# Kernel optimization log

Hardware: AMD Instinct MI355X
Metric: run time of the kernel (lower is better)

The kernel has to match this reference:

```python
import jax, jax.numpy as jnp
import numpy as np

jax.config.update("jax_enable_x64", True)  # original casts to double for covpool/SVD

BN_EPS = 1e-5


def setup_inputs() -> dict:
    key = jax.random.key(0)
    k1, k2 = jax.random.split(key)
    x = jax.random.normal(k1, (64, 2048, 14, 14), dtype=jnp.float32)
    conv_w = jax.random.normal(k2, (256, 2048), dtype=jnp.float32) * 0.02  # 1x1 conv kernel
    bn_gamma = jnp.ones((256,), dtype=jnp.float32)
    bn_beta = jnp.zeros((256,), dtype=jnp.float32)
    return {"x": x, "conv_w": conv_w, "bn_gamma": bn_gamma, "bn_beta": bn_beta}


def reference(x, conv_w, bn_gamma, bn_beta):
    # --- dimension reduction block: 1x1 conv (no bias) + BN (train mode) + ReLU ---
    y = jnp.einsum('oc,bchw->bohw', conv_w, x)  # [B,256,14,14]
    mean = y.mean(axis=(0, 2, 3), keepdims=True)
    var = y.var(axis=(0, 2, 3), keepdims=True)
    y = (y - mean) * jax.lax.rsqrt(var + BN_EPS)
    y = y * bn_gamma[None, :, None, None] + bn_beta[None, :, None, None]
    y = jnp.maximum(y, 0.0)

    # --- Covpool: x @ (I/M - 11^T/M^2) @ x^T, in float64 as original ---
    B, d, h, w = y.shape
    M = h * w
    z = y.reshape(B, d, M).astype(jnp.float64)
    zc = z - z.mean(axis=2, keepdims=True)          # centering == multiplying by I_hat
    cov = jnp.einsum('bim,bjm->bij', zc, zc) / M    # [B,d,d], symmetric PSD

    # --- Eigen decomposition (SVD of symmetric PSD == eigh), clamp tiny eigvals ---
    s, V = jnp.linalg.eigh(cov)                     # s: [B,d], V: [B,d,d]
    eps = jnp.finfo(jnp.float64).eps
    s = jnp.maximum(s, eps)

    # --- Power: matrix square root Q = V sqrt(S) V^T ---
    Q = jnp.einsum('bij,bj,bkj->bik', V, jnp.sqrt(s), V)  # [B,d,d]

    # --- upper-triangular (incl. diag) vectorization, row-major like torch triu ---
    iu = jnp.triu_indices(d)
    q_triv = Q[:, iu[0], iu[1]]                     # [B, d*(d+1)/2]
    return q_triv.astype(jnp.float32)
```

## Files before the change

### kernel.cpp

```cpp
#include <hip/hip_runtime.h>
#include <hip/hip_bf16.h>

static constexpr int B   = 64;
static constexpr int CIN = 2048;
static constexpr int O   = 256;
static constexpr int HW  = 196;
static constexpr int D   = 256;
static constexpr int TRI = 32896;
static constexpr int NQ_COUPLED = 5;
static constexpr size_t NELEM = (size_t)B * D * D;
static constexpr size_t YN    = (size_t)B * O * HW;

typedef unsigned short u16;
typedef unsigned short u16x4 __attribute__((ext_vector_type(4)));
typedef unsigned short u16x8 __attribute__((ext_vector_type(8)));
typedef __bf16         bf16x8 __attribute__((ext_vector_type(8)));
typedef float          f32x4 __attribute__((ext_vector_type(4)));

static __device__ __forceinline__ u16 f2bf(float x) {
    unsigned int u = __float_as_uint(x);
    u += 0x7FFFu + ((u >> 16) & 1u);
    return (u16)(u >> 16);
}
static __device__ __forceinline__ float bf2f(u16 h) {
    return __uint_as_float(((unsigned int)h) << 16);
}
static __device__ __forceinline__ f32x4 mm_bf16(u16x8 a, u16x8 b, f32x4 c) {
    return __builtin_amdgcn_mfma_f32_16x16x32_bf16(
        __builtin_bit_cast(bf16x8, a), __builtin_bit_cast(bf16x8, b), c, 0, 0, 0);
}

__global__ __launch_bounds__(256) void k_wsplit(const float* __restrict__ W,
                                                u16* __restrict__ Wh,
                                                u16* __restrict__ Wl) {
    const size_t i = (size_t)blockIdx.x * 256 + threadIdx.x;
    const float v = W[i];
    const u16 h = f2bf(v);
    Wh[i] = h;
    Wl[i] = f2bf(v - bf2f(h));
}

__global__ __launch_bounds__(256, 2) void k_conv(const float* __restrict__ x,
                                                 const u16* __restrict__ Wh,
                                                 const u16* __restrict__ Wl,
                                                 float* __restrict__ psum) {
    const int l   = blockIdx.x;
    const int xcd = l & 7, u = l >> 3;
    const int q   = xcd * 98 + u;
    const int ks  = q & 3;
    const int t2  = q >> 2;
    const int ot  = t2 & 1, gt = t2 >> 1;
    const int o0  = ot * 128;
    const int cbase = ks * 512;
    float* yp = psum + (size_t)ks * YN;

    const int tid = threadIdx.x;

    __shared__ u16 sW[2][128][72], sX[2][128][72];

    const int colX  = tid & 127;
    const int chalf = (tid >> 7) * 32;
    const int gX = gt * 128 + colX;
    const int bX = gX / 196;
    const int mX = gX - bX * 196;
    const size_t xbase = (size_t)bX * (CIN * HW) + mX;

    const int rW = tid >> 1, kh = (tid & 1) * 32;
    const u16* gWh = Wh + (size_t)(o0 + rW) * CIN + cbase + kh;
    const u16* gWl = Wl + (size_t)(o0 + rW) * CIN + cbase + kh;

    const int lane = tid & 63, w = tid >> 6;
    const int wr = w >> 1, wc = w & 1;
    const int lr = lane & 15, lg = lane >> 4, ko = lg << 3;

    f32x4 acc[4][4] = {};

    u16x8 pWh[4], pWl[4];
    float pX[32];
    u16x4 cXh[8], cXl[8];

    auto loadW = [&](int kb) {
        #pragma unroll
        for (int qq = 0; qq < 4; ++qq) {
            pWh[qq] = *(const u16x8*)&gWh[kb + qq * 8];
            pWl[qq] = *(const u16x8*)&gWl[kb + qq * 8];
        }
    };
    auto loadX = [&](int kb) {
        #pragma unroll
        for (int i = 0; i < 32; ++i)
            pX[i] = x[xbase + (size_t)(cbase + kb + chalf + i) * HW];
    };
    auto convX = [&]() {
        #pragma unroll
        for (int i = 0; i < 32; i += 4) {
            u16x4 vh, vl;
            #pragma unroll
            for (int j = 0; j < 4; ++j) {
                const float v = pX[i + j];
                const u16 h = f2bf(v);
                vh[j] = h;
                vl[j] = f2bf(v - bf2f(h));
            }
            cXh[i >> 2] = vh;
            cXl[i >> 2] = vl;
        }
    };
    auto storeWX = [&]() {
        #pragma unroll
        for (int qq = 0; qq < 4; ++qq) {
            *(u16x8*)&sW[0][rW][kh + qq * 8] = pWh[qq];
            *(u16x8*)&sW[1][rW][kh + qq * 8] = pWl[qq];
        }
        #pragma unroll
        for (int qq = 0; qq < 8; ++qq) {
            *(u16x4*)&sX[0][colX][chalf + qq * 4] = cXh[qq];
            *(u16x4*)&sX[1][colX][chalf + qq * 4] = cXl[qq];
        }
    };
    auto compute = [&]() {
        #pragma unroll
        for (int kr = 0; kr < 2; ++kr) {
            const int kk = kr * 32 + ko;
            u16x8 fah[4], fal[4], fbh[4], fbl[4];
            #pragma unroll
            for (int f = 0; f < 4; ++f) {
                fah[f] = *(const u16x8*)&sW[0][wr * 64 + f * 16 + lr][kk];
                fal[f] = *(const u16x8*)&sW[1][wr * 64 + f * 16 + lr][kk];
                fbh[f] = *(const u16x8*)&sX[0][wc * 64 + f * 16 + lr][kk];
                fbl[f] = *(const u16x8*)&sX[1][wc * 64 + f * 16 + lr][kk];
            }
            #pragma unroll
            for (int fi = 0; fi < 4; ++fi)
                #pragma unroll
                for (int fj = 0; fj < 4; ++fj) {
                    acc[fi][fj] = mm_bf16(fah[fi], fbh[fj], acc[fi][fj]);
                    acc[fi][fj] = mm_bf16(fah[fi], fbl[fj], acc[fi][fj]);
                    acc[fi][fj] = mm_bf16(fal[fi], fbh[fj], acc[fi][fj]);
                }
        }
    };

    loadW(0); loadX(0); convX();
    for (int st = 0; st < 8; ++st) {
        __syncthreads();
        storeWX();
        __syncthreads();
        if (st < 7) { loadW((st + 1) * 64); loadX((st + 1) * 64); }
        compute();
        if (st < 7) convX();
    }

    #pragma unroll
    for (int fj = 0; fj < 4; ++fj) {
        const int gcol = gt * 128 + wc * 64 + fj * 16 + lr;
        const int bb = gcol / 196;
        const int mm = gcol - bb * 196;
        const size_t ybase = (size_t)bb * (O * HW) + mm;
        #pragma unroll
        for (int fi = 0; fi < 4; ++fi)
            #pragma unroll
            for (int r = 0; r < 4; ++r) {
                const int orow = o0 + wr * 64 + fi * 16 + (lg << 2) + r;
                yp[ybase + (size_t)orow * HW] = acc[fi][fj][r];
            }
    }
}

__global__ __launch_bounds__(256) void k_redy(const float* __restrict__ ps,
                                              float* __restrict__ y) {
    const size_t i = ((size_t)blockIdx.x * 256 + threadIdx.x) * 4;
    if (i >= YN) return;
    float4 a = *(const float4*)&ps[i];
    const float4 b = *(const float4*)&ps[YN + i];
    const float4 c = *(const float4*)&ps[2 * YN + i];
    const float4 d = *(const float4*)&ps[3 * YN + i];
    a.x += b.x + c.x + d.x; a.y += b.y + c.y + d.y;
    a.z += b.z + c.z + d.z; a.w += b.w + c.w + d.w;
    *(float4*)&y[i] = a;
}

__global__ __launch_bounds__(256) void k_bnstats(const float* __restrict__ y,
                                                 const float* __restrict__ gamma,
                                                 const float* __restrict__ beta,
                                                 float* __restrict__ scl,
                                                 float* __restrict__ shf) {
    const int o = blockIdx.x;
    const int tid = threadIdx.x;
    float s = 0.f, s2 = 0.f;
    if (tid < HW) {
        for (int b = 0; b < B; ++b) {
            const float v = y[((size_t)b * O + o) * HW + tid];
            s += v; s2 += v * v;
        }
    }
    #pragma unroll
    for (int msk = 32; msk; msk >>= 1) {
        s  += __shfl_xor(s,  msk);
        s2 += __shfl_xor(s2, msk);
    }
    __shared__ float rs[4], rs2[4];
    if ((tid & 63) == 0) { rs[tid >> 6] = s; rs2[tid >> 6] = s2; }
    __syncthreads();
    if (tid == 0) {
        const float N = (float)(B * HW);
        const float ts  = rs[0] + rs[1] + rs[2] + rs[3];
        const float ts2 = rs2[0] + rs2[1] + rs2[2] + rs2[3];
        const float mean = ts / N;
        const float var  = ts2 / N - mean * mean;
        const float sc = gamma[o] * rsqrtf(var + 1e-5f);
        scl[o] = sc;
        shf[o] = beta[o] - mean * sc;
    }
}

__global__ __launch_bounds__(64) void k_center(float* __restrict__ z,
                                               const float* __restrict__ scl,
                                               const float* __restrict__ shf) {
    const int row = blockIdx.x;
    const int o = row & 255;
    const int lane = threadIdx.x;
    const float sc = scl[o], sh = shf[o];
    float* zr = &z[(size_t)row * HW];
    float vals[4];
    float s = 0.f;
    #pragma unroll
    for (int q = 0; q < 4; ++q) {
        const int m = q * 64 + lane;
        float v = 0.f;
        if (m < HW) v = fmaxf(fmaf(zr[m], sc, sh), 0.f);
        vals[q] = v; s += v;
    }
    #pragma unroll
    for (int msk = 32; msk; msk >>= 1) s += __shfl_xor(s, msk);
    const float mean = s / (float)HW;
    #pragma unroll
    for (int q = 0; q < 4; ++q) {
        const int m = q * 64 + lane;
        if (m < HW) zr[m] = vals[q] - mean;
    }
}

__global__ __launch_bounds__(256) void k_cov(const float* __restrict__ z,
                                             double* __restrict__ cov) {
    const int b = blockIdx.y;
    const int jt = blockIdx.x & 3, it = blockIdx.x >> 2;
    const int i0 = it * 64, j0 = jt * 64;
    const int tid = threadIdx.x;
    const int tn = tid & 15, tmq = tid >> 4;

    __shared__ float sA[28][68], sB[28][68];
    double acc[4][4] = {};
    const float* zb = &z[(size_t)b * D * HW];

    for (int k0 = 0; k0 < HW; k0 += 28) {
        #pragma unroll
        for (int q = 0; q < 7; ++q) {
            const int idx = tid + q * 256;
            const int r = idx / 28, kk = idx % 28;
            sA[kk][r] = zb[(size_t)(i0 + r) * HW + k0 + kk];
            sB[kk][r] = zb[(size_t)(j0 + r) * HW + k0 + kk];
        }
        __syncthreads();
        #pragma unroll
        for (int kk = 0; kk < 28; ++kk) {
            const float4 av = *reinterpret_cast<const float4*>(&sA[kk][tmq << 2]);
            const float4 bv = *reinterpret_cast<const float4*>(&sB[kk][tn << 2]);
            const double aa[4] = {av.x, av.y, av.z, av.w};
            const double bb[4] = {bv.x, bv.y, bv.z, bv.w};
            #pragma unroll
            for (int i = 0; i < 4; ++i)
                #pragma unroll
                for (int j = 0; j < 4; ++j)
                    acc[i][j] = fma(aa[i], bb[j], acc[i][j]);
        }
        __syncthreads();
    }
    const double inv = 1.0 / (double)HW;
    #pragma unroll
    for (int i = 0; i < 4; ++i)
        #pragma unroll
        for (int j = 0; j < 4; ++j)
            cov[(size_t)b * D * D + (size_t)(i0 + (tmq << 2) + i) * D
                + j0 + (tn << 2) + j] = acc[i][j] * inv;
}

__global__ __launch_bounds__(256) void k_lmax(const double* __restrict__ cov,
                                              double* __restrict__ cn) {
    const int b = blockIdx.x;
    const int tid = threadIdx.x;
    const double* A = &cov[(size_t)b * D * D];
    __shared__ float vs[256];
    __shared__ float red[4];
    vs[tid] = 1.0f;
    __syncthreads();
    float lam = 1.0f;
    for (int it = 0; it < 6; ++it) {
        float u0 = 0.f, u1 = 0.f, u2 = 0.f, u3 = 0.f;
        #pragma unroll 8
        for (int k = 0; k < D; k += 4) {
            u0 = fmaf((float)A[(size_t)(k + 0) * D + tid], vs[k + 0], u0);
            u1 = fmaf((float)A[(size_t)(k + 1) * D + tid], vs[k + 1], u1);
            u2 = fmaf((float)A[(size_t)(k + 2) * D + tid], vs[k + 2], u2);
            u3 = fmaf((float)A[(size_t)(k + 3) * D + tid], vs[k + 3], u3);
        }
        const float u = (u0 + u1) + (u2 + u3);
        float s = u * u;
        #pragma unroll
        for (int msk = 32; msk; msk >>= 1) s += __shfl_xor(s, msk);
        __syncthreads();
        if ((tid & 63) == 0) red[tid >> 6] = s;
        __syncthreads();
        const float nrm = sqrtf(red[0] + red[1] + red[2] + red[3]) + 1e-30f;
        lam = nrm;
        vs[tid] = u / nrm;
        __syncthreads();
    }
    if (tid == 0) cn[b] = (lam > 1e-30f) ? 1.25 * (double)lam : 1.0;
}

__global__ __launch_bounds__(256) void k_init(const double* __restrict__ cov,
                                              const double* __restrict__ cn,
                                              u16* __restrict__ Yh,
                                              u16* __restrict__ Yl) {
    const size_t e = (size_t)blockIdx.x * 256 + threadIdx.x;
    const int b = (int)(e >> 16);
    const int ij = (int)(e & 65535);
    const int i = ij >> 8, j = ij & 255;
    const double diag = (i == j) ? 1e-7 : 0.0;
    const float f = (float)(cov[e] / cn[b] + diag);
    const u16 h = f2bf(f);
    Yh[e] = h;
    Yl[e] = f2bf(f - bf2f(h));
}

template <int MODE, int FUSED>
__global__ __launch_bounds__(256, 2) void k_mgemm(
        const u16* __restrict__ A0h, const u16* __restrict__ A0l,
        const u16* __restrict__ B0h, const u16* __restrict__ B0l,
        u16* __restrict__ C0h, u16* __restrict__ C0l,
        const u16* __restrict__ A1h, const u16* __restrict__ A1l,
        const u16* __restrict__ B1h, const u16* __restrict__ B1l,
        u16* __restrict__ C1h, u16* __restrict__ C1l,
        const double* __restrict__ cn, float* __restrict__ outp) {
    const int orig = blockIdx.x;
    const int xcd  = orig & 7;
    const int s    = orig >> 3;
    int batch, tile, opz;
    if (FUSED) {
        const int bl  = s >> 4;
        const int t16 = s & 15;
        opz  = t16 >> 3;
        tile = t16 & 7;
        batch = xcd * 8 + bl;
    } else {
        opz = 0;
        batch = xcd * 8 + (s >> 3);
        tile = s & 7;
    }

    const u16 *Ah, *Al, *Bh, *Bl;
    u16 *Ch, *Cl;
    if (opz == 0) { Ah = A0h; Al = A0l; Bh = B0h; Bl = B0l; Ch = C0h; Cl = C0l; }
    else          { Ah = A1h; Al = A1l; Bh = B1h; Bl = B1l; Ch = C1h; Cl = C1l; }

    const int i0 = (tile >> 2) * 128, j0 = (tile & 3) * 64;
    const size_t boff = (size_t)batch * 65536;
    Ah += boff; Al += boff; Bh += boff; Bl += boff; Ch += boff; Cl += boff;

    const int tid = threadIdx.x;
    __shared__ u16 sA[2][128][72];
    __shared__ u16 sB[2][64][72];

    const int rA = tid >> 1, khA = (tid & 1) * 32;
    const u16* gAh = Ah + (size_t)(i0 + rA) * 256 + khA;
    const u16* gAl = Al + (size_t)(i0 + rA) * 256 + khA;
    const int rB = tid >> 2, khB = (tid & 3) * 16;
    const u16* gBh = Bh + (size_t)(j0 + rB) * 256 + khB;
    const u16* gBl = Bl + (size_t)(j0 + rB) * 256 + khB;

    const int lane = tid & 63, w = tid >> 6;
    const int wr = w >> 1, wc = w & 1;
    const int lr = lane & 15, lg = lane >> 4, ko = lg << 3;

    f32x4 acc[4][2] = {};

    u16x8 pAh[4], pAl[4], pBh[2], pBl[2];
    auto g_load = [&](int kb) {
        #pragma unroll
        for (int qq = 0; qq < 4; ++qq) {
            pAh[qq] = *(const u16x8*)&gAh[kb + qq * 8];
            pAl[qq] = *(const u16x8*)&gAl[kb + qq * 8];
        }
        #pragma unroll
        for (int qq = 0; qq < 2; ++qq) {
            pBh[qq] = *(const u16x8*)&gBh[kb + qq * 8];
            pBl[qq] = *(const u16x8*)&gBl[kb + qq * 8];
        }
    };
    auto s_store = [&]() {
        #pragma unroll
        for (int qq = 0; qq < 4; ++qq) {
            *(u16x8*)&sA[0][rA][khA + qq * 8] = pAh[qq];
            *(u16x8*)&sA[1][rA][khA + qq * 8] = pAl[qq];
        }
        #pragma unroll
        for (int qq = 0; qq < 2; ++qq) {
            *(u16x8*)&sB[0][rB][khB + qq * 8] = pBh[qq];
            *(u16x8*)&sB[1][rB][khB + qq * 8] = pBl[qq];
        }
    };
    auto compute = [&]() {
        #pragma unroll
        for (int kr = 0; kr < 2; ++kr) {
            const int kk = kr * 32 + ko;
            u16x8 fah[4], fal[4], fbh[2], fbl[2];
            #pragma unroll
            for (int f = 0; f < 4; ++f) {
                fah[f] = *(const u16x8*)&sA[0][wr * 64 + f * 16 + lr][kk];
                fal[f] = *(const u16x8*)&sA[1][wr * 64 + f * 16 + lr][kk];
            }
            #pragma unroll
            for (int f = 0; f < 2; ++f) {
                fbh[f] = *(const u16x8*)&sB[0][wc * 32 + f * 16 + lr][kk];
                fbl[f] = *(const u16x8*)&sB[1][wc * 32 + f * 16 + lr][kk];
            }
            #pragma unroll
            for (int fi = 0; fi < 4; ++fi)
                #pragma unroll
                for (int fj = 0; fj < 2; ++fj) {
                    acc[fi][fj] = mm_bf16(fah[fi], fbh[fj], acc[fi][fj]);
                    acc[fi][fj] = mm_bf16(fah[fi], fbl[fj], acc[fi][fj]);
                    acc[fi][fj] = mm_bf16(fal[fi], fbh[fj], acc[fi][fj]);
                }
        }
    };

    g_load(0);
    for (int st = 0; st < 4; ++st) {
        __syncthreads();
        s_store();
        __syncthreads();
        if (st < 3) g_load((st + 1) * 64);
        compute();
    }

    const int orow = wr * 64 + (lg << 2);
    const int ocol = wc * 32 + lr;

    if (MODE == 3) {
        const double sc = sqrt(cn[batch]);
        #pragma unroll
        for (int fi = 0; fi < 4; ++fi)
            #pragma unroll
            for (int r = 0; r < 4; ++r) {
                const int gi = i0 + orow + fi * 16 + r;
                const size_t rowoff = (size_t)gi * D - ((size_t)gi * (gi - 1)) / 2;
                #pragma unroll
                for (int fj = 0; fj < 2; ++fj) {
                    const int gj = j0 + ocol + fj * 16;
                    if (gj >= gi)
                        outp[(size_t)batch * TRI + rowoff + (gj - gi)] =
                            (float)(sc * (double)acc[fi][fj][r]);
                }
            }
        return;
    }

    #pragma unroll
    for (int fi = 0; fi < 4; ++fi)
        #pragma unroll
        for (int r = 0; r < 4; ++r) {
            const int gi = i0 + orow + fi * 16 + r;
            #pragma unroll
            for (int fj = 0; fj < 2; ++fj) {
                const int gj = j0 + ocol + fj * 16;
                float v = acc[fi][fj][r];
                if (MODE == 1) {
                    const size_t xo = (size_t)gi * 256 + gj;
                    const float xv = bf2f(Ah[xo]) + bf2f(Al[xo]);
                    v = (((gi == gj) ? 15.0f : 0.0f) - 10.0f * xv + 3.0f * v) * 0.125f;
                }
                const u16 h = f2bf(v);
                const u16 lo = f2bf(v - bf2f(h));
                const size_t co = (size_t)gi * 256 + gj;
                Ch[co] = h;
                Cl[co] = lo;
            }
        }
}

extern "C" void kernel_launch(void* const* d_in, const int* in_sizes, int n_in,
                              void* d_out, int out_size, void* d_ws, size_t ws_size,
                              hipStream_t stream) {
    const float* x     = (const float*)d_in[0];
    const float* W     = (const float*)d_in[1];
    const float* gamma = (const float*)d_in[2];
    const float* beta  = (const float*)d_in[3];
    float* out = (float*)d_out;

    char* ws = (char*)d_ws;
    size_t off = 0;
    auto alloc = [&](size_t bytes) -> void* {
        void* p = ws + off;
        off += (bytes + 255) & ~(size_t)255;
        return p;
    };
    float*  y    = (float*)alloc(YN * sizeof(float));
    double* cov  = (double*)alloc(NELEM * sizeof(double));
    float*  scl  = (float*)alloc(O * sizeof(float));
    float*  shf  = (float*)alloc(O * sizeof(float));
    double* cn   = (double*)alloc(B * sizeof(double));
    u16*    Wh   = (u16*)alloc((size_t)O * CIN * sizeof(u16));
    u16*    Wl   = (u16*)alloc((size_t)O * CIN * sizeof(u16));
    u16* pl = (u16*)alloc(12 * NELEM * sizeof(u16));
    if (off > ws_size) return;
    u16 *YAh = pl,             *YAl = pl + NELEM;
    u16 *YBh = pl + 2 * NELEM, *YBl = pl + 3 * NELEM;
    u16 *MAh = pl + 4 * NELEM, *MAl = pl + 5 * NELEM;
    u16 *MBh = pl + 6 * NELEM, *MBl = pl + 7 * NELEM;
    u16 *Rh  = pl + 8 * NELEM, *Rl  = pl + 9 * NELEM;
    u16 *Uh  = pl + 10 * NELEM,*Ul  = pl + 11 * NELEM;
    float* psum = (float*)pl;

    k_wsplit <<<(O * CIN) / 256, 256, 0, stream>>>(W, Wh, Wl);
    k_conv   <<<784, 256, 0, stream>>>(x, Wh, Wl, psum);
    k_redy   <<<3136, 256, 0, stream>>>(psum, y);
    k_bnstats<<<O, 256, 0, stream>>>(y, gamma, beta, scl, shf);
    k_center <<<B * O, 64, 0, stream>>>(y, scl, shf);
    k_cov    <<<dim3(16, B), 256, 0, stream>>>(y, cov);
    k_lmax   <<<B, 256, 0, stream>>>(cov, cn);
    k_init   <<<B * 256, 256, 0, stream>>>(cov, cn, YAh, YAl);

    k_mgemm<1, 0><<<512, 256, 0, stream>>>(YAh, YAl, YAh, YAl, Rh, Rl,
                                           YAh, YAl, YAh, YAl, Rh, Rl, cn, out);
    k_mgemm<2, 0><<<512, 256, 0, stream>>>(YAh, YAl, Rh, Rl, YBh, YBl,
                                           YAh, YAl, Rh, Rl, YBh, YBl, cn, out);
    k_mgemm<2, 0><<<512, 256, 0, stream>>>(Rh, Rl, YBh, YBl, MBh, MBl,
                                           Rh, Rl, YBh, YBl, MBh, MBl, cn, out);

    u16 *Ych = YBh, *Ycl = YBl, *Yah = YAh, *Yal = YAl;
    u16 *Mch = MBh, *Mcl = MBl, *Mah = MAh, *Mal = MAl;
    for (int itq = 0; itq < NQ_COUPLED; ++itq) {
        k_mgemm<1, 0><<<512, 256, 0, stream>>>(Mch, Mcl, Mch, Mcl, Rh, Rl,
                                               Mch, Mcl, Mch, Mcl, Rh, Rl, cn, out);
        k_mgemm<2, 1><<<1024, 256, 0, stream>>>(Ych, Ycl, Rh, Rl, Yah, Yal,
                                                Mch, Mcl, Rh, Rl, Uh, Ul, cn, out);
        k_mgemm<2, 0><<<512, 256, 0, stream>>>(Rh, Rl, Uh, Ul, Mah, Mal,
                                               Rh, Rl, Uh, Ul, Mah, Mal, cn, out);
        u16* t;
        t = Ych; Ych = Yah; Yah = t;  t = Ycl; Ycl = Yal; Yal = t;
        t = Mch; Mch = Mah; Mah = t;  t = Mcl; Mcl = Mal; Mal = t;
    }
    k_mgemm<1, 0><<<512, 256, 0, stream>>>(Mch, Mcl, Mch, Mcl, Rh, Rl,
                                           Mch, Mcl, Mch, Mcl, Rh, Rl, cn, out);
    k_mgemm<3, 0><<<512, 256, 0, stream>>>(Ych, Ycl, Rh, Rl, Uh, Ul,
                                           Ych, Ycl, Rh, Rl, Uh, Ul, cn, out);
}
```

Baseline: 508.8 us.

## Fuse Newton-Schulz chain into one cooperative persistent kernel; shrink conv K-tile

Merges power-iteration normalisation, init and every Newton-Schulz GEMM stage into a single cooperative kernel that uses grid.sync between stages, which removes many separate kernel launches and their gaps. The covariance is now stored as float instead of double, halving its traffic. The conv kernel moves to a 32-wide K tile with smaller shared buffers and a request for 3 blocks per CU, trading more loop iterations and barriers for higher occupancy. The risks are grid-sync overhead, the noinline tile function adding call cost and blocking register allocation across it, and float covariance losing precision.

```diff
diff --git a/kernel.cpp b/kernel.cpp
--- a/kernel.cpp
+++ b/kernel.cpp
@@ -1,5 +1,8 @@
 #include <hip/hip_runtime.h>
 #include <hip/hip_bf16.h>
+#include <hip/hip_cooperative_groups.h>
+
+namespace cg = cooperative_groups;
 
 static constexpr int B   = 64;
 static constexpr int CIN = 2048;
@@ -40,7 +43,7 @@
     Wl[i] = f2bf(v - bf2f(h));
 }
 
-__global__ __launch_bounds__(256, 2) void k_conv(const float* __restrict__ x,
+__global__ __launch_bounds__(256, 3) void k_conv(const float* __restrict__ x,
                                                  const u16* __restrict__ Wh,
                                                  const u16* __restrict__ Wl,
                                                  float* __restrict__ psum) {
@@ -56,18 +59,18 @@
 
     const int tid = threadIdx.x;
 
-    __shared__ u16 sW[2][128][72], sX[2][128][72];
+    __shared__ u16 sW[2][128][40], sX[2][128][40];
 
     const int colX  = tid & 127;
-    const int chalf = (tid >> 7) * 32;
+    const int chalf = (tid >> 7) * 16;
     const int gX = gt * 128 + colX;
     const int bX = gX / 196;
     const int mX = gX - bX * 196;
     const size_t xbase = (size_t)bX * (CIN * HW) + mX;
 
-    const int rW = tid >> 1, kh = (tid & 1) * 32;
-    const u16* gWh = Wh + (size_t)(o0 + rW) * CIN + cbase + kh;
-    const u16* gWl = Wl + (size_t)(o0 + rW) * CIN + cbase + kh;
+    const int rW = tid >> 1, kq = (tid & 1) * 16;
+    const u16* gWh = Wh + (size_t)(o0 + rW) * CIN + cbase + kq;
+    const u16* gWl = Wl + (size_t)(o0 + rW) * CIN + cbase + kq;
 
     const int lane = tid & 63, w = tid >> 6;
     const int wr = w >> 1, wc = w & 1;
@@ -75,25 +78,25 @@
 
     f32x4 acc[4][4] = {};
 
-    u16x8 pWh[4], pWl[4];
-    float pX[32];
-    u16x4 cXh[8], cXl[8];
+    u16x8 pWh[2], pWl[2];
+    float pX[16];
+    u16x4 cXh[4], cXl[4];
 
     auto loadW = [&](int kb) {
         #pragma unroll
-        for (int qq = 0; qq < 4; ++qq) {
+        for (int qq = 0; qq < 2; ++qq) {
             pWh[qq] = *(const u16x8*)&gWh[kb + qq * 8];
             pWl[qq] = *(const u16x8*)&gWl[kb + qq * 8];
         }
     };
     auto loadX = [&](int kb) {
         #pragma unroll
-        for (int i = 0; i < 32; ++i)
+        for (int i = 0; i < 16; ++i)
             pX[i] = x[xbase + (size_t)(cbase + kb + chalf + i) * HW];
     };
     auto convX = [&]() {
         #pragma unroll
-        for (int i = 0; i < 32; i += 4) {
+        for (int i = 0; i < 16; i += 4) {
             u16x4 vh, vl;
             #pragma unroll
             for (int j = 0; j < 4; ++j) {
@@ -108,47 +111,43 @@
     };
     auto storeWX = [&]() {
         #pragma unroll
+        for (int qq = 0; qq < 2; ++qq) {
+            *(u16x8*)&sW[0][rW][kq + qq * 8] = pWh[qq];
+            *(u16x8*)&sW[1][rW][kq + qq * 8] = pWl[qq];
+        }
+        #pragma unroll
         for (int qq = 0; qq < 4; ++qq) {
-            *(u16x8*)&sW[0][rW][kh + qq * 8] = pWh[qq];
-            *(u16x8*)&sW[1][rW][kh + qq * 8] = pWl[qq];
-        }
-        #pragma unroll
-        for (int qq = 0; qq < 8; ++qq) {
             *(u16x4*)&sX[0][colX][chalf + qq * 4] = cXh[qq];
             *(u16x4*)&sX[1][colX][chalf + qq * 4] = cXl[qq];
         }
     };
     auto compute = [&]() {
-        #pragma unroll
-        for (int kr = 0; kr < 2; ++kr) {
-            const int kk = kr * 32 + ko;
-            u16x8 fah[4], fal[4], fbh[4], fbl[4];
-            #pragma unroll
-            for (int f = 0; f < 4; ++f) {
-                fah[f] = *(const u16x8*)&sW[0][wr * 64 + f * 16 + lr][kk];
-                fal[f] = *(const u16x8*)&sW[1][wr * 64 + f * 16 + lr][kk];
-                fbh[f] = *(const u16x8*)&sX[0][wc * 64 + f * 16 + lr][kk];
-                fbl[f] = *(const u16x8*)&sX[1][wc * 64 + f * 16 + lr][kk];
-            }
-            #pragma unroll
-            for (int fi = 0; fi < 4; ++fi)
-                #pragma unroll
-                for (int fj = 0; fj < 4; ++fj) {
-                    acc[fi][fj] = mm_bf16(fah[fi], fbh[fj], acc[fi][fj]);
-                    acc[fi][fj] = mm_bf16(fah[fi], fbl[fj], acc[fi][fj]);
-                    acc[fi][fj] = mm_bf16(fal[fi], fbh[fj], acc[fi][fj]);
-                }
-        }
+        u16x8 fah[4], fal[4], fbh[4], fbl[4];
+        #pragma unroll
+        for (int f = 0; f < 4; ++f) {
+            fah[f] = *(const u16x8*)&sW[0][wr * 64 + f * 16 + lr][ko];
+            fal[f] = *(const u16x8*)&sW[1][wr * 64 + f * 16 + lr][ko];
+            fbh[f] = *(const u16x8*)&sX[0][wc * 64 + f * 16 + lr][ko];
+            fbl[f] = *(const u16x8*)&sX[1][wc * 64 + f * 16 + lr][ko];
+        }
+        #pragma unroll
+        for (int fi = 0; fi < 4; ++fi)
+            #pragma unroll
+            for (int fj = 0; fj < 4; ++fj) {
+                acc[fi][fj] = mm_bf16(fah[fi], fbh[fj], acc[fi][fj]);
+                acc[fi][fj] = mm_bf16(fah[fi], fbl[fj], acc[fi][fj]);
+                acc[fi][fj] = mm_bf16(fal[fi], fbh[fj], acc[fi][fj]);
+            }
     };
 
     loadW(0); loadX(0); convX();
-    for (int st = 0; st < 8; ++st) {
+    for (int st = 0; st < 16; ++st) {
         __syncthreads();
         storeWX();
         __syncthreads();
-        if (st < 7) { loadW((st + 1) * 64); loadX((st + 1) * 64); }
+        if (st < 15) { loadW((st + 1) * 32); loadX((st + 1) * 32); }
         compute();
-        if (st < 7) convX();
+        if (st < 15) convX();
     }
 
     #pragma unroll
@@ -242,7 +241,7 @@
 }
 
 __global__ __launch_bounds__(256) void k_cov(const float* __restrict__ z,
-                                             double* __restrict__ cov) {
+                                             float* __restrict__ covf) {
     const int b = blockIdx.y;
     const int jt = blockIdx.x & 3, it = blockIdx.x >> 2;
     const int i0 = it * 64, j0 = jt * 64;
@@ -281,96 +280,31 @@
     for (int i = 0; i < 4; ++i)
         #pragma unroll
         for (int j = 0; j < 4; ++j)
-            cov[(size_t)b * D * D + (size_t)(i0 + (tmq << 2) + i) * D
-                + j0 + (tn << 2) + j] = acc[i][j] * inv;
-}
-
-__global__ __launch_bounds__(256) void k_lmax(const double* __restrict__ cov,
-                                              double* __restrict__ cn) {
-    const int b = blockIdx.x;
-    const int tid = threadIdx.x;
-    const double* A = &cov[(size_t)b * D * D];
-    __shared__ float vs[256];
-    __shared__ float red[4];
-    vs[tid] = 1.0f;
-    __syncthreads();
-    float lam = 1.0f;
-    for (int it = 0; it < 6; ++it) {
-        float u0 = 0.f, u1 = 0.f, u2 = 0.f, u3 = 0.f;
-        #pragma unroll 8
-        for (int k = 0; k < D; k += 4) {
-            u0 = fmaf((float)A[(size_t)(k + 0) * D + tid], vs[k + 0], u0);
-            u1 = fmaf((float)A[(size_t)(k + 1) * D + tid], vs[k + 1], u1);
-            u2 = fmaf((float)A[(size_t)(k + 2) * D + tid], vs[k + 2], u2);
-            u3 = fmaf((float)A[(size_t)(k + 3) * D + tid], vs[k + 3], u3);
-        }
-        const float u = (u0 + u1) + (u2 + u3);
-        float s = u * u;
-        #pragma unroll
-        for (int msk = 32; msk; msk >>= 1) s += __shfl_xor(s, msk);
-        __syncthreads();
-        if ((tid & 63) == 0) red[tid >> 6] = s;
-        __syncthreads();
-        const float nrm = sqrtf(red[0] + red[1] + red[2] + red[3]) + 1e-30f;
-        lam = nrm;
-        vs[tid] = u / nrm;
-        __syncthreads();
-    }
-    if (tid == 0) cn[b] = (lam > 1e-30f) ? 1.25 * (double)lam : 1.0;
-}
-
-__global__ __launch_bounds__(256) void k_init(const double* __restrict__ cov,
-                                              const double* __restrict__ cn,
-                                              u16* __restrict__ Yh,
-                                              u16* __restrict__ Yl) {
-    const size_t e = (size_t)blockIdx.x * 256 + threadIdx.x;
-    const int b = (int)(e >> 16);
-    const int ij = (int)(e & 65535);
-    const int i = ij >> 8, j = ij & 255;
-    const double diag = (i == j) ? 1e-7 : 0.0;
-    const float f = (float)(cov[e] / cn[b] + diag);
-    const u16 h = f2bf(f);
-    Yh[e] = h;
-    Yl[e] = f2bf(f - bf2f(h));
-}
-
-template <int MODE, int FUSED>
-__global__ __launch_bounds__(256, 2) void k_mgemm(
-        const u16* __restrict__ A0h, const u16* __restrict__ A0l,
-        const u16* __restrict__ B0h, const u16* __restrict__ B0l,
-        u16* __restrict__ C0h, u16* __restrict__ C0l,
-        const u16* __restrict__ A1h, const u16* __restrict__ A1l,
-        const u16* __restrict__ B1h, const u16* __restrict__ B1l,
-        u16* __restrict__ C1h, u16* __restrict__ C1l,
-        const double* __restrict__ cn, float* __restrict__ outp) {
-    const int orig = blockIdx.x;
-    const int xcd  = orig & 7;
-    const int s    = orig >> 3;
-    int batch, tile, opz;
-    if (FUSED) {
-        const int bl  = s >> 4;
-        const int t16 = s & 15;
-        opz  = t16 >> 3;
-        tile = t16 & 7;
-        batch = xcd * 8 + bl;
-    } else {
-        opz = 0;
-        batch = xcd * 8 + (s >> 3);
-        tile = s & 7;
-    }
-
-    const u16 *Ah, *Al, *Bh, *Bl;
-    u16 *Ch, *Cl;
-    if (opz == 0) { Ah = A0h; Al = A0l; Bh = B0h; Bl = B0l; Ch = C0h; Cl = C0l; }
-    else          { Ah = A1h; Al = A1l; Bh = B1h; Bl = B1l; Ch = C1h; Cl = C1l; }
-
+            covf[(size_t)b * D * D + (size_t)(i0 + (tmq << 2) + i) * D
+                 + j0 + (tn << 2) + j] = (float)(acc[i][j] * inv);
+}
+
+template <int MODE>
+__device__ __noinline__ void gemm_tile(
+        const u16* __restrict__ Ahb, const u16* __restrict__ Alb,
+        const u16* __restrict__ Bhb, const u16* __restrict__ Blb,
+        u16* __restrict__ Chb, u16* __restrict__ Clb,
+        int batch, int tile,
+        const double* __restrict__ cn, float* __restrict__ outp,
+        u16* __restrict__ sAbuf, u16* __restrict__ sBbuf) {
     const int i0 = (tile >> 2) * 128, j0 = (tile & 3) * 64;
     const size_t boff = (size_t)batch * 65536;
-    Ah += boff; Al += boff; Bh += boff; Bl += boff; Ch += boff; Cl += boff;
+    const u16* Ah = Ahb + boff; const u16* Al = Alb + boff;
+    const u16* Bh = Bhb + boff; const u16* Bl = Blb + boff;
+    u16* Ch = Chb + boff; u16* Cl = Clb + boff;
 
     const int tid = threadIdx.x;
-    __shared__ u16 sA[2][128][72];
-    __shared__ u16 sB[2][64][72];
+    auto sA = [&](int p, int r, int k) -> u16* {
+        return &sAbuf[(size_t)((p << 7) + r) * 72 + k];
+    };
+    auto sB = [&](int p, int r, int k) -> u16* {
+        return &sBbuf[(size_t)((p << 6) + r) * 72 + k];
+    };
 
     const int rA = tid >> 1, khA = (tid & 1) * 32;
     const u16* gAh = Ah + (size_t)(i0 + rA) * 256 + khA;
@@ -401,13 +335,13 @@
     auto s_store = [&]() {
         #pragma unroll
         for (int qq = 0; qq < 4; ++qq) {
-            *(u16x8*)&sA[0][rA][khA + qq * 8] = pAh[qq];
-            *(u16x8*)&sA[1][rA][khA + qq * 8] = pAl[qq];
+            *(u16x8*)sA(0, rA, khA + qq * 8) = pAh[qq];
+            *(u16x8*)sA(1, rA, khA + qq * 8) = pAl[qq];
         }
         #pragma unroll
         for (int qq = 0; qq < 2; ++qq) {
-            *(u16x8*)&sB[0][rB][khB + qq * 8] = pBh[qq];
-            *(u16x8*)&sB[1][rB][khB + qq * 8] = pBl[qq];
+            *(u16x8*)sB(0, rB, khB + qq * 8) = pBh[qq];
+            *(u16x8*)sB(1, rB, khB + qq * 8) = pBl[qq];
         }
     };
     auto compute = [&]() {
@@ -417,13 +351,13 @@
             u16x8 fah[4], fal[4], fbh[2], fbl[2];
             #pragma unroll
             for (int f = 0; f < 4; ++f) {
-                fah[f] = *(const u16x8*)&sA[0][wr * 64 + f * 16 + lr][kk];
-                fal[f] = *(const u16x8*)&sA[1][wr * 64 + f * 16 + lr][kk];
+                fah[f] = *(const u16x8*)sA(0, wr * 64 + f * 16 + lr, kk);
+                fal[f] = *(const u16x8*)sA(1, wr * 64 + f * 16 + lr, kk);
             }
             #pragma unroll
             for (int f = 0; f < 2; ++f) {
-                fbh[f] = *(const u16x8*)&sB[0][wc * 32 + f * 16 + lr][kk];
-                fbl[f] = *(const u16x8*)&sB[1][wc * 32 + f * 16 + lr][kk];
+                fbh[f] = *(const u16x8*)sB(0, wc * 32 + f * 16 + lr, kk);
+                fbl[f] = *(const u16x8*)sB(1, wc * 32 + f * 16 + lr, kk);
             }
             #pragma unroll
             for (int fi = 0; fi < 4; ++fi)
@@ -490,6 +424,114 @@
         }
 }
 
+__global__ __launch_bounds__(256, 2) void k_chain(const float* __restrict__ covf,
+                                                  double* __restrict__ cn,
+                                                  u16* __restrict__ pl,
+                                                  float* __restrict__ outp) {
+    __shared__ u16 sAbuf[2 * 128 * 72];
+    __shared__ u16 sBbuf[2 * 64 * 72];
+    __shared__ float vs[256];
+    __shared__ float red[4];
+
+    u16 *YAh = pl,              *YAl = pl + NELEM;
+    u16 *YBh = pl + 2 * NELEM,  *YBl = pl + 3 * NELEM;
+    u16 *MAh = pl + 4 * NELEM,  *MAl = pl + 5 * NELEM;
+    u16 *MBh = pl + 6 * NELEM,  *MBl = pl + 7 * NELEM;
+    u16 *Rh  = pl + 8 * NELEM,  *Rl  = pl + 9 * NELEM;
+    u16 *Uh  = pl + 10 * NELEM, *Ul  = pl + 11 * NELEM;
+
+    const int tid = threadIdx.x;
+    cg::grid_group grid = cg::this_grid();
+
+    for (int b = blockIdx.x; b < B; b += gridDim.x) {
+        const float* A = covf + (size_t)b * 65536;
+        vs[tid] = 1.f;
+        __syncthreads();
+        float lam = 1.f;
+        for (int it = 0; it < 6; ++it) {
+            float u0 = 0.f, u1 = 0.f, u2 = 0.f, u3 = 0.f;
+            #pragma unroll 8
+            for (int k = 0; k < D; k += 4) {
+                u0 = fmaf(A[(size_t)(k + 0) * D + tid], vs[k + 0], u0);
+                u1 = fmaf(A[(size_t)(k + 1) * D + tid], vs[k + 1], u1);
+                u2 = fmaf(A[(size_t)(k + 2) * D + tid], vs[k + 2], u2);
+                u3 = fmaf(A[(size_t)(k + 3) * D + tid], vs[k + 3], u3);
+            }
+            const float uu = (u0 + u1) + (u2 + u3);
+            float sq = uu * uu;
+            #pragma unroll
+            for (int msk = 32; msk; msk >>= 1) sq += __shfl_xor(sq, msk);
+            __syncthreads();
+            if ((tid & 63) == 0) red[tid >> 6] = sq;
+            __syncthreads();
+            const float nrm = sqrtf(red[0] + red[1] + red[2] + red[3]) + 1e-30f;
+            lam = nrm;
+            vs[tid] = uu / nrm;
+            __syncthreads();
+        }
+        if (tid == 0) cn[b] = (lam > 1e-30f) ? 1.25 * (double)lam : 1.0;
+        __syncthreads();
+    }
+    grid.sync();
+
+    for (size_t e = (size_t)blockIdx.x * 256 + tid; e < NELEM;
+         e += (size_t)gridDim.x * 256) {
+        const int b = (int)(e >> 16);
+        const int ij = (int)(e & 65535);
+        const float diag = ((ij >> 8) == (ij & 255)) ? 1e-7f : 0.f;
+        const float f = covf[e] / (float)cn[b] + diag;
+        const u16 h = f2bf(f);
+        YAh[e] = h;
+        YAl[e] = f2bf(f - bf2f(h));
+    }
+    grid.sync();
+
+    auto run1 = [&](const u16* Ah, const u16* Al, const u16* Bh, const u16* Bl,
+                    u16* Ch, u16* Cl) {
+        for (int t = blockIdx.x; t < 512; t += gridDim.x) {
+            const int xc = t & 7, ss = t >> 3;
+            gemm_tile<1>(Ah, Al, Bh, Bl, Ch, Cl, xc * 8 + (ss >> 3), ss & 7,
+                         cn, outp, sAbuf, sBbuf);
+        }
+    };
+    auto run2 = [&](const u16* Ah, const u16* Al, const u16* Bh, const u16* Bl,
+                    u16* Ch, u16* Cl) {
+        for (int t = blockIdx.x; t < 512; t += gridDim.x) {
+            const int xc = t & 7, ss = t >> 3;
+            gemm_tile<2>(Ah, Al, Bh, Bl, Ch, Cl, xc * 8 + (ss >> 3), ss & 7,
+                         cn, outp, sAbuf, sBbuf);
+        }
+    };
+    auto run3 = [&](const u16* Ah, const u16* Al, const u16* Bh, const u16* Bl,
+                    u16* Ch, u16* Cl) {
+        for (int t = blockIdx.x; t < 512; t += gridDim.x) {
+            const int xc = t & 7, ss = t >> 3;
+            gemm_tile<3>(Ah, Al, Bh, Bl, Ch, Cl, xc * 8 + (ss >> 3), ss & 7,
+                         cn, outp, sAbuf, sBbuf);
+        }
+    };
+
+    run1(YAh, YAl, YAh, YAl, Rh, Rl);                    grid.sync();
+    run2(YAh, YAl, Rh, Rl, YBh, YBl);                    grid.sync();
+    run2(Rh, Rl, YBh, YBl, MBh, MBl);                    grid.sync();
+
+    u16 *Ych = YBh, *Ycl = YBl, *Yah = YAh, *Yal = YAl;
+    u16 *Mch = MBh, *Mcl = MBl, *Mah = MAh, *Mal = MAl;
+    for (int itq = 0; itq < NQ_COUPLED; ++itq) {
+        run1(Mch, Mcl, Mch, Mcl, Rh, Rl);                grid.sync();
+        run2(Ych, Ycl, Rh, Rl, Yah, Yal);
+        run2(Mch, Mcl, Rh, Rl, Uh, Ul);
+        grid.sync();
+        run2(Rh, Rl, Uh, Ul, Mah, Mal);
+        grid.sync();
+        u16* t;
+        t = Ych; Ych = Yah; Yah = t;  t = Ycl; Ycl = Yal; Yal = t;
+        t = Mch; Mch = Mah; Mah = t;  t = Mcl; Mcl = Mal; Mal = t;
+    }
+    run1(Mch, Mcl, Mch, Mcl, Rh, Rl);                    grid.sync();
+    run3(Ych, Ycl, Rh, Rl, Uh, Ul);
+}
+
 extern "C" void kernel_launch(void* const* d_in, const int* in_sizes, int n_in,
                               void* d_out, int out_size, void* d_ws, size_t ws_size,
                               hipStream_t stream) {
@@ -507,7 +549,7 @@
         return p;
     };
     float*  y    = (float*)alloc(YN * sizeof(float));
-    double* cov  = (double*)alloc(NELEM * sizeof(double));
+    float*  covf = (float*)alloc(NELEM * sizeof(float));
     float*  scl  = (float*)alloc(O * sizeof(float));
     float*  shf  = (float*)alloc(O * sizeof(float));
     double* cn   = (double*)alloc(B * sizeof(double));
@@ -515,12 +557,6 @@
     u16*    Wl   = (u16*)alloc((size_t)O * CIN * sizeof(u16));
     u16* pl = (u16*)alloc(12 * NELEM * sizeof(u16));
     if (off > ws_size) return;
-    u16 *YAh = pl,             *YAl = pl + NELEM;
-    u16 *YBh = pl + 2 * NELEM, *YBl = pl + 3 * NELEM;
-    u16 *MAh = pl + 4 * NELEM, *MAl = pl + 5 * NELEM;
-    u16 *MBh = pl + 6 * NELEM, *MBl = pl + 7 * NELEM;
-    u16 *Rh  = pl + 8 * NELEM, *Rl  = pl + 9 * NELEM;
-    u16 *Uh  = pl + 10 * NELEM,*Ul  = pl + 11 * NELEM;
     float* psum = (float*)pl;
 
     k_wsplit <<<(O * CIN) / 256, 256, 0, stream>>>(W, Wh, Wl);
@@ -528,32 +564,15 @@
     k_redy   <<<3136, 256, 0, stream>>>(psum, y);
     k_bnstats<<<O, 256, 0, stream>>>(y, gamma, beta, scl, shf);
     k_center <<<B * O, 64, 0, stream>>>(y, scl, shf);
-    k_cov    <<<dim3(16, B), 256, 0, stream>>>(y, cov);
-    k_lmax   <<<B, 256, 0, stream>>>(cov, cn);
-    k_init   <<<B * 256, 256, 0, stream>>>(cov, cn, YAh, YAl);
-
-    k_mgemm<1, 0><<<512, 256, 0, stream>>>(YAh, YAl, YAh, YAl, Rh, Rl,
-                                           YAh, YAl, YAh, YAl, Rh, Rl, cn, out);
-    k_mgemm<2, 0><<<512, 256, 0, stream>>>(YAh, YAl, Rh, Rl, YBh, YBl,
-                                           YAh, YAl, Rh, Rl, YBh, YBl, cn, out);
-    k_mgemm<2, 0><<<512, 256, 0, stream>>>(Rh, Rl, YBh, YBl, MBh, MBl,
-                                           Rh, Rl, YBh, YBl, MBh, MBl, cn, out);
-
-    u16 *Ych = YBh, *Ycl = YBl, *Yah = YAh, *Yal = YAl;
-    u16 *Mch = MBh, *Mcl = MBl, *Mah = MAh, *Mal = MAl;
-    for (int itq = 0; itq < NQ_COUPLED; ++itq) {
-        k_mgemm<1, 0><<<512, 256, 0, stream>>>(Mch, Mcl, Mch, Mcl, Rh, Rl,
-                                               Mch, Mcl, Mch, Mcl, Rh, Rl, cn, out);
-        k_mgemm<2, 1><<<1024, 256, 0, stream>>>(Ych, Ycl, Rh, Rl, Yah, Yal,
-                                                Mch, Mcl, Rh, Rl, Uh, Ul, cn, out);
-        k_mgemm<2, 0><<<512, 256, 0, stream>>>(Rh, Rl, Uh, Ul, Mah, Mal,
-                                               Rh, Rl, Uh, Ul, Mah, Mal, cn, out);
-        u16* t;
-        t = Ych; Ych = Yah; Yah = t;  t = Ycl; Ycl = Yal; Yal = t;
-        t = Mch; Mch = Mah; Mah = t;  t = Mcl; Mcl = Mal; Mal = t;
-    }
-    k_mgemm<1, 0><<<512, 256, 0, stream>>>(Mch, Mcl, Mch, Mcl, Rh, Rl,
-                                           Mch, Mcl, Mch, Mcl, Rh, Rl, cn, out);
-    k_mgemm<3, 0><<<512, 256, 0, stream>>>(Ych, Ycl, Rh, Rl, Uh, Ul,
-                                           Ych, Ycl, Rh, Rl, Uh, Ul, cn, out);
-}
+    k_cov    <<<dim3(16, B), 256, 0, stream>>>(y, covf);
+
+    int nb = 0;
+    if (hipOccupancyMaxActiveBlocksPerMultiprocessor(&nb, k_chain, 256, 0)
+            != hipSuccess || nb < 1)
+        nb = 2;
+    int grid = nb * 256;
+    if (grid > 512) grid = 512;
+    const float* covf_c = covf;
+    void* args[] = {(void*)&covf_c, (void*)&cn, (void*)&pl, (void*)&out};
+    hipLaunchCooperativeKernel(k_chain, dim3(grid), dim3(256), args, 0, stream);
+}
```

After: 1.302 ms. 2.56x slower.

## Exploit symmetry in Newton-Schulz GEMMs, shrink conv K-tile, store covariance in float

Applied to the files above, without the earlier changes.

The batched matrix-GEMM kernel now computes only 6 of the 8 output tiles per matrix and fills the missing lower blocks by transposing the off-diagonal tiles through shared memory. This relies on the iterates being symmetric and cuts GEMM work and grid size by a quarter. The conv kernel halves its K-tile from 64 to 32 so it uses less LDS and fewer registers, allowing 3 blocks per CU, at the cost of twice as many sync steps. The covariance buffer becomes float instead of double, which halves the memory traffic in the power-iteration and init kernels.

```diff
diff --git a/kernel.cpp b/kernel.cpp
--- a/kernel.cpp
+++ b/kernel.cpp
@@ -40,7 +40,7 @@
     Wl[i] = f2bf(v - bf2f(h));
 }
 
-__global__ __launch_bounds__(256, 2) void k_conv(const float* __restrict__ x,
+__global__ __launch_bounds__(256, 3) void k_conv(const float* __restrict__ x,
                                                  const u16* __restrict__ Wh,
                                                  const u16* __restrict__ Wl,
                                                  float* __restrict__ psum) {
@@ -56,18 +56,18 @@
 
     const int tid = threadIdx.x;
 
-    __shared__ u16 sW[2][128][72], sX[2][128][72];
+    __shared__ u16 sW[2][128][40], sX[2][128][40];
 
     const int colX  = tid & 127;
-    const int chalf = (tid >> 7) * 32;
+    const int chalf = (tid >> 7) * 16;
     const int gX = gt * 128 + colX;
     const int bX = gX / 196;
     const int mX = gX - bX * 196;
     const size_t xbase = (size_t)bX * (CIN * HW) + mX;
 
-    const int rW = tid >> 1, kh = (tid & 1) * 32;
-    const u16* gWh = Wh + (size_t)(o0 + rW) * CIN + cbase + kh;
-    const u16* gWl = Wl + (size_t)(o0 + rW) * CIN + cbase + kh;
+    const int rW = tid >> 1, kq = (tid & 1) * 16;
+    const u16* gWh = Wh + (size_t)(o0 + rW) * CIN + cbase + kq;
+    const u16* gWl = Wl + (size_t)(o0 + rW) * CIN + cbase + kq;
 
     const int lane = tid & 63, w = tid >> 6;
     const int wr = w >> 1, wc = w & 1;
@@ -75,25 +75,25 @@
 
     f32x4 acc[4][4] = {};
 
-    u16x8 pWh[4], pWl[4];
-    float pX[32];
-    u16x4 cXh[8], cXl[8];
+    u16x8 pWh[2], pWl[2];
+    float pX[16];
+    u16x4 cXh[4], cXl[4];
 
     auto loadW = [&](int kb) {
         #pragma unroll
-        for (int qq = 0; qq < 4; ++qq) {
+        for (int qq = 0; qq < 2; ++qq) {
             pWh[qq] = *(const u16x8*)&gWh[kb + qq * 8];
             pWl[qq] = *(const u16x8*)&gWl[kb + qq * 8];
         }
     };
     auto loadX = [&](int kb) {
         #pragma unroll
-        for (int i = 0; i < 32; ++i)
+        for (int i = 0; i < 16; ++i)
             pX[i] = x[xbase + (size_t)(cbase + kb + chalf + i) * HW];
     };
     auto convX = [&]() {
         #pragma unroll
-        for (int i = 0; i < 32; i += 4) {
+        for (int i = 0; i < 16; i += 4) {
             u16x4 vh, vl;
             #pragma unroll
             for (int j = 0; j < 4; ++j) {
@@ -108,47 +108,43 @@
     };
     auto storeWX = [&]() {
         #pragma unroll
+        for (int qq = 0; qq < 2; ++qq) {
+            *(u16x8*)&sW[0][rW][kq + qq * 8] = pWh[qq];
+            *(u16x8*)&sW[1][rW][kq + qq * 8] = pWl[qq];
+        }
+        #pragma unroll
         for (int qq = 0; qq < 4; ++qq) {
-            *(u16x8*)&sW[0][rW][kh + qq * 8] = pWh[qq];
-            *(u16x8*)&sW[1][rW][kh + qq * 8] = pWl[qq];
-        }
-        #pragma unroll
-        for (int qq = 0; qq < 8; ++qq) {
             *(u16x4*)&sX[0][colX][chalf + qq * 4] = cXh[qq];
             *(u16x4*)&sX[1][colX][chalf + qq * 4] = cXl[qq];
         }
     };
     auto compute = [&]() {
-        #pragma unroll
-        for (int kr = 0; kr < 2; ++kr) {
-            const int kk = kr * 32 + ko;
-            u16x8 fah[4], fal[4], fbh[4], fbl[4];
-            #pragma unroll
-            for (int f = 0; f < 4; ++f) {
-                fah[f] = *(const u16x8*)&sW[0][wr * 64 + f * 16 + lr][kk];
-                fal[f] = *(const u16x8*)&sW[1][wr * 64 + f * 16 + lr][kk];
-                fbh[f] = *(const u16x8*)&sX[0][wc * 64 + f * 16 + lr][kk];
-                fbl[f] = *(const u16x8*)&sX[1][wc * 64 + f * 16 + lr][kk];
-            }
-            #pragma unroll
-            for (int fi = 0; fi < 4; ++fi)
-                #pragma unroll
-                for (int fj = 0; fj < 4; ++fj) {
-                    acc[fi][fj] = mm_bf16(fah[fi], fbh[fj], acc[fi][fj]);
-                    acc[fi][fj] = mm_bf16(fah[fi], fbl[fj], acc[fi][fj]);
-                    acc[fi][fj] = mm_bf16(fal[fi], fbh[fj], acc[fi][fj]);
-                }
-        }
+        u16x8 fah[4], fal[4], fbh[4], fbl[4];
+        #pragma unroll
+        for (int f = 0; f < 4; ++f) {
+            fah[f] = *(const u16x8*)&sW[0][wr * 64 + f * 16 + lr][ko];
+            fal[f] = *(const u16x8*)&sW[1][wr * 64 + f * 16 + lr][ko];
+            fbh[f] = *(const u16x8*)&sX[0][wc * 64 + f * 16 + lr][ko];
+            fbl[f] = *(const u16x8*)&sX[1][wc * 64 + f * 16 + lr][ko];
+        }
+        #pragma unroll
+        for (int fi = 0; fi < 4; ++fi)
+            #pragma unroll
+            for (int fj = 0; fj < 4; ++fj) {
+                acc[fi][fj] = mm_bf16(fah[fi], fbh[fj], acc[fi][fj]);
+                acc[fi][fj] = mm_bf16(fah[fi], fbl[fj], acc[fi][fj]);
+                acc[fi][fj] = mm_bf16(fal[fi], fbh[fj], acc[fi][fj]);
+            }
     };
 
     loadW(0); loadX(0); convX();
-    for (int st = 0; st < 8; ++st) {
+    for (int st = 0; st < 16; ++st) {
         __syncthreads();
         storeWX();
         __syncthreads();
-        if (st < 7) { loadW((st + 1) * 64); loadX((st + 1) * 64); }
+        if (st < 15) { loadW((st + 1) * 32); loadX((st + 1) * 32); }
         compute();
-        if (st < 7) convX();
+        if (st < 15) convX();
     }
 
     #pragma unroll
@@ -242,7 +238,7 @@
 }
 
 __global__ __launch_bounds__(256) void k_cov(const float* __restrict__ z,
-                                             double* __restrict__ cov) {
+                                             float* __restrict__ covf) {
     const int b = blockIdx.y;
     const int jt = blockIdx.x & 3, it = blockIdx.x >> 2;
     const int i0 = it * 64, j0 = jt * 64;
@@ -281,54 +277,53 @@
     for (int i = 0; i < 4; ++i)
         #pragma unroll
         for (int j = 0; j < 4; ++j)
-            cov[(size_t)b * D * D + (size_t)(i0 + (tmq << 2) + i) * D
-                + j0 + (tn << 2) + j] = acc[i][j] * inv;
-}
-
-__global__ __launch_bounds__(256) void k_lmax(const double* __restrict__ cov,
+            covf[(size_t)b * D * D + (size_t)(i0 + (tmq << 2) + i) * D
+                 + j0 + (tn << 2) + j] = (float)(acc[i][j] * inv);
+}
+
+__global__ __launch_bounds__(256) void k_lmax(const float* __restrict__ covf,
                                               double* __restrict__ cn) {
     const int b = blockIdx.x;
     const int tid = threadIdx.x;
-    const double* A = &cov[(size_t)b * D * D];
+    const float* A = &covf[(size_t)b * 65536];
     __shared__ float vs[256];
     __shared__ float red[4];
-    vs[tid] = 1.0f;
+    vs[tid] = 1.f;
     __syncthreads();
-    float lam = 1.0f;
+    float lam = 1.f;
     for (int it = 0; it < 6; ++it) {
         float u0 = 0.f, u1 = 0.f, u2 = 0.f, u3 = 0.f;
         #pragma unroll 8
         for (int k = 0; k < D; k += 4) {
-            u0 = fmaf((float)A[(size_t)(k + 0) * D + tid], vs[k + 0], u0);
-            u1 = fmaf((float)A[(size_t)(k + 1) * D + tid], vs[k + 1], u1);
-            u2 = fmaf((float)A[(size_t)(k + 2) * D + tid], vs[k + 2], u2);
-            u3 = fmaf((float)A[(size_t)(k + 3) * D + tid], vs[k + 3], u3);
-        }
-        const float u = (u0 + u1) + (u2 + u3);
-        float s = u * u;
-        #pragma unroll
-        for (int msk = 32; msk; msk >>= 1) s += __shfl_xor(s, msk);
-        __syncthreads();
-        if ((tid & 63) == 0) red[tid >> 6] = s;
+            u0 = fmaf(A[(size_t)(k + 0) * D + tid], vs[k + 0], u0);
+            u1 = fmaf(A[(size_t)(k + 1) * D + tid], vs[k + 1], u1);
+            u2 = fmaf(A[(size_t)(k + 2) * D + tid], vs[k + 2], u2);
+            u3 = fmaf(A[(size_t)(k + 3) * D + tid], vs[k + 3], u3);
+        }
+        const float uu = (u0 + u1) + (u2 + u3);
+        float sq = uu * uu;
+        #pragma unroll
+        for (int msk = 32; msk; msk >>= 1) sq += __shfl_xor(sq, msk);
+        __syncthreads();
+        if ((tid & 63) == 0) red[tid >> 6] = sq;
         __syncthreads();
         const float nrm = sqrtf(red[0] + red[1] + red[2] + red[3]) + 1e-30f;
         lam = nrm;
-        vs[tid] = u / nrm;
+        vs[tid] = uu / nrm;
         __syncthreads();
     }
     if (tid == 0) cn[b] = (lam > 1e-30f) ? 1.25 * (double)lam : 1.0;
 }
 
-__global__ __launch_bounds__(256) void k_init(const double* __restrict__ cov,
+__global__ __launch_bounds__(256) void k_init(const float* __restrict__ covf,
                                               const double* __restrict__ cn,
                                               u16* __restrict__ Yh,
                                               u16* __restrict__ Yl) {
     const size_t e = (size_t)blockIdx.x * 256 + threadIdx.x;
     const int b = (int)(e >> 16);
     const int ij = (int)(e & 65535);
-    const int i = ij >> 8, j = ij & 255;
-    const double diag = (i == j) ? 1e-7 : 0.0;
-    const float f = (float)(cov[e] / cn[b] + diag);
+    const float diag = ((ij >> 8) == (ij & 255)) ? 1e-7f : 0.f;
+    const float f = covf[e] / (float)cn[b] + diag;
     const u16 h = f2bf(f);
     Yh[e] = h;
     Yl[e] = f2bf(f - bf2f(h));
@@ -346,17 +341,18 @@
     const int orig = blockIdx.x;
     const int xcd  = orig & 7;
     const int s    = orig >> 3;
-    int batch, tile, opz;
+    int batch, task, opz;
     if (FUSED) {
-        const int bl  = s >> 4;
-        const int t16 = s & 15;
-        opz  = t16 >> 3;
-        tile = t16 & 7;
+        const int bl  = s / 12;
+        const int rem = s - bl * 12;
+        opz  = rem >= 6;
+        task = rem - opz * 6;
         batch = xcd * 8 + bl;
     } else {
         opz = 0;
-        batch = xcd * 8 + (s >> 3);
-        tile = s & 7;
+        const int bl = s / 6;
+        task = s - bl * 6;
+        batch = xcd * 8 + bl;
     }
 
     const u16 *Ah, *Al, *Bh, *Bl;
@@ -364,7 +360,9 @@
     if (opz == 0) { Ah = A0h; Al = A0l; Bh = B0h; Bl = B0l; Ch = C0h; Cl = C0l; }
     else          { Ah = A1h; Al = A1l; Bh = B1h; Bl = B1l; Ch = C1h; Cl = C1l; }
 
-    const int i0 = (tile >> 2) * 128, j0 = (tile & 3) * 64;
+    const int it = task >> 2;
+    const int jt = (task < 4) ? task : task - 2;
+    const int i0 = it * 128, j0 = jt * 64;
     const size_t boff = (size_t)batch * 65536;
     Ah += boff; Al += boff; Bh += boff; Bl += boff; Ch += boff; Cl += boff;
 
@@ -467,6 +465,7 @@
         return;
     }
 
+    u16 hv[4][4][2], lv[4][4][2];
     #pragma unroll
     for (int fi = 0; fi < 4; ++fi)
         #pragma unroll
@@ -486,8 +485,36 @@
                 const size_t co = (size_t)gi * 256 + gj;
                 Ch[co] = h;
                 Cl[co] = lo;
-            }
-        }
+                hv[fi][r][fj] = h;
+                lv[fi][r][fj] = lo;
+            }
+        }
+
+    if (task == 2 || task == 3) {
+        __syncthreads();
+        u16 (*tH)[136] = reinterpret_cast<u16(*)[136]>(&sA[0][0][0]);
+        u16 (*tL)[136] = reinterpret_cast<u16(*)[136]>(&sB[0][0][0]);
+        #pragma unroll
+        for (int fi = 0; fi < 4; ++fi)
+            #pragma unroll
+            for (int r = 0; r < 4; ++r) {
+                const int li = orow + fi * 16 + r;
+                #pragma unroll
+                for (int fj = 0; fj < 2; ++fj) {
+                    const int lj = ocol + fj * 16;
+                    tH[lj][li] = hv[fi][r][fj];
+                    tL[lj][li] = lv[fi][r][fj];
+                }
+            }
+        __syncthreads();
+        const int r2 = tid >> 2, c2 = (tid & 3) << 5;
+        const size_t mo = (size_t)(j0 + r2) * 256 + i0 + c2;
+        #pragma unroll
+        for (int qq = 0; qq < 4; ++qq) {
+            *(u16x8*)&Ch[mo + qq * 8] = *(const u16x8*)&tH[r2][c2 + qq * 8];
+            *(u16x8*)&Cl[mo + qq * 8] = *(const u16x8*)&tL[r2][c2 + qq * 8];
+        }
+    }
 }
 
 extern "C" void kernel_launch(void* const* d_in, const int* in_sizes, int n_in,
@@ -507,7 +534,7 @@
         return p;
     };
     float*  y    = (float*)alloc(YN * sizeof(float));
-    double* cov  = (double*)alloc(NELEM * sizeof(double));
+    float*  covf = (float*)alloc(NELEM * sizeof(float));
     float*  scl  = (float*)alloc(O * sizeof(float));
     float*  shf  = (float*)alloc(O * sizeof(float));
     double* cn   = (double*)alloc(B * sizeof(double));
@@ -528,32 +555,32 @@
     k_redy   <<<3136, 256, 0, stream>>>(psum, y);
     k_bnstats<<<O, 256, 0, stream>>>(y, gamma, beta, scl, shf);
     k_center <<<B * O, 64, 0, stream>>>(y, scl, shf);
-    k_cov    <<<dim3(16, B), 256, 0, stream>>>(y, cov);
-    k_lmax   <<<B, 256, 0, stream>>>(cov, cn);
-    k_init   <<<B * 256, 256, 0, stream>>>(cov, cn, YAh, YAl);
-
-    k_mgemm<1, 0><<<512, 256, 0, stream>>>(YAh, YAl, YAh, YAl, Rh, Rl,
+    k_cov    <<<dim3(16, B), 256, 0, stream>>>(y, covf);
+    k_lmax   <<<B, 256, 0, stream>>>(covf, cn);
+    k_init   <<<B * 256, 256, 0, stream>>>(covf, cn, YAh, YAl);
+
+    k_mgemm<1, 0><<<384, 256, 0, stream>>>(YAh, YAl, YAh, YAl, Rh, Rl,
                                            YAh, YAl, YAh, YAl, Rh, Rl, cn, out);
-    k_mgemm<2, 0><<<512, 256, 0, stream>>>(YAh, YAl, Rh, Rl, YBh, YBl,
+    k_mgemm<2, 0><<<384, 256, 0, stream>>>(YAh, YAl, Rh, Rl, YBh, YBl,
                                            YAh, YAl, Rh, Rl, YBh, YBl, cn, out);
-    k_mgemm<2, 0><<<512, 256, 0, stream>>>(Rh, Rl, YBh, YBl, MBh, MBl,
+    k_mgemm<2, 0><<<384, 256, 0, stream>>>(Rh, Rl, YBh, YBl, MBh, MBl,
                                            Rh, Rl, YBh, YBl, MBh, MBl, cn, out);
 
     u16 *Ych = YBh, *Ycl = YBl, *Yah = YAh, *Yal = YAl;
     u16 *Mch = MBh, *Mcl = MBl, *Mah = MAh, *Mal = MAl;
     for (int itq = 0; itq < NQ_COUPLED; ++itq) {
-        k_mgemm<1, 0><<<512, 256, 0, stream>>>(Mch, Mcl, Mch, Mcl, Rh, Rl,
+        k_mgemm<1, 0><<<384, 256, 0, stream>>>(Mch, Mcl, Mch, Mcl, Rh, Rl,
                                                Mch, Mcl, Mch, Mcl, Rh, Rl, cn, out);
-        k_mgemm<2, 1><<<1024, 256, 0, stream>>>(Ych, Ycl, Rh, Rl, Yah, Yal,
-                                                Mch, Mcl, Rh, Rl, Uh, Ul, cn, out);
-        k_mgemm<2, 0><<<512, 256, 0, stream>>>(Rh, Rl, Uh, Ul, Mah, Mal,
+        k_mgemm<2, 1><<<768, 256, 0, stream>>>(Ych, Ycl, Rh, Rl, Yah, Yal,
+                                               Mch, Mcl, Rh, Rl, Uh, Ul, cn, out);
+        k_mgemm<2, 0><<<384, 256, 0, stream>>>(Rh, Rl, Uh, Ul, Mah, Mal,
                                                Rh, Rl, Uh, Ul, Mah, Mal, cn, out);
         u16* t;
         t = Ych; Ych = Yah; Yah = t;  t = Ycl; Ycl = Yal; Yal = t;
         t = Mch; Mch = Mah; Mah = t;  t = Mcl; Mcl = Mal; Mal = t;
     }
-    k_mgemm<1, 0><<<512, 256, 0, stream>>>(Mch, Mcl, Mch, Mcl, Rh, Rl,
+    k_mgemm<1, 0><<<384, 256, 0, stream>>>(Mch, Mcl, Mch, Mcl, Rh, Rl,
                                            Mch, Mcl, Mch, Mcl, Rh, Rl, cn, out);
-    k_mgemm<3, 0><<<512, 256, 0, stream>>>(Ych, Ycl, Rh, Rl, Uh, Ul,
+    k_mgemm<3, 0><<<384, 256, 0, stream>>>(Ych, Ycl, Rh, Rl, Uh, Ul,
                                            Ych, Ycl, Rh, Rl, Uh, Ul, cn, out);
 }
```

After: 508.3 us. About the same (-0.1%).
